# Kernel optimization log

Hardware: AMD Instinct MI355X
Metric: run time of the kernel (lower is better)

Reference implementation:

```python
import jax, jax.numpy as jnp
import numpy as np

EPS = 1e-05


def layer_norm(x, scale):
    # Faithful to source bug: returns scale * x_norm + scale (shift param unused)
    mean = jnp.mean(x, axis=-1, keepdims=True)
    var = jnp.var(x, axis=-1, keepdims=True)  # unbiased=False
    x_norm = (x - mean) / jnp.sqrt(var + EPS)
    return scale * x_norm + scale


def mhsa(x, wq, wk, wv, wo, bo, n_heads):
    b, t, d = x.shape
    hd = d // n_heads
    # torch Linear: y = x @ W.T (no qkv bias)
    q = (x @ wq.T).reshape(b, t, n_heads, hd).transpose(0, 2, 1, 3)  # bhtd
    k = (x @ wk.T).reshape(b, t, n_heads, hd).transpose(0, 2, 1, 3)
    v = (x @ wv.T).reshape(b, t, n_heads, hd).transpose(0, 2, 1, 3)
    scores = jnp.einsum('bhqd,bhkd->bhqk', q, k)
    causal = jnp.triu(jnp.ones((t, t), dtype=bool), k=1)
    scores = jnp.where(causal, -jnp.inf, scores)
    attn = jax.nn.softmax(scores / np.sqrt(hd).astype(np.float32), axis=-1)
    ctx = jnp.einsum('bhqk,bhkd->bhqd', attn, v)
    ctx = ctx.transpose(0, 2, 1, 3).reshape(b, t, d)
    return ctx @ wo.T + bo


def setup_inputs() -> dict:
    key = jax.random.key(0)
    ks = jax.random.split(key, 6)
    B, T, D = 2, 2048, 1024
    return {
        'x': jax.random.normal(ks[0], (B, T, D), dtype=jnp.float32),
        'wq': jax.random.normal(ks[1], (D, D), dtype=jnp.float32) * 0.02,
        'wk': jax.random.normal(ks[2], (D, D), dtype=jnp.float32) * 0.02,
        'wv': jax.random.normal(ks[3], (D, D), dtype=jnp.float32) * 0.02,
        'wo': jax.random.normal(ks[4], (D, D), dtype=jnp.float32) * 0.02,
        'bo': jnp.zeros((D,), dtype=jnp.float32),
        'ln1_scale': jnp.ones((D,), dtype=jnp.float32),
        'ln2_scale': jnp.ones((D,), dtype=jnp.float32),
    }


def reference(x, wq, wk, wv, wo, bo, ln1_scale, ln2_scale):
    n_heads = 16
    # Block 1: norm1 -> attn -> (+residual); dropout is identity in eval mode
    h = x + mhsa(layer_norm(x, ln1_scale), wq, wk, wv, wo, bo, n_heads)
    # Block 2: source calls self.attn (same weights) again, not self.ff
    out = h + mhsa(layer_norm(h, ln2_scale), wq, wk, wv, wo, bo, n_heads)
    return out
```

## Files before the change

kernel.cpp:

```cpp
#include <hip/hip_runtime.h>
#include <hip/hip_bf16.h>
#include <math.h>

#define Dm 1024
#define Tm 2048
#define Bm 2
#define Hm 16
#define HDm 64
#define Rm (Bm*Tm)
#define QS 3072

typedef __attribute__((ext_vector_type(8))) short sh8;
typedef __attribute__((ext_vector_type(4))) float f32x4;

#define AS1(p) ((const __attribute__((address_space(1))) void*)(p))
#define AS3(p) ((__attribute__((address_space(3))) void*)(p))

__device__ __forceinline__ short f2bs(float f) {
    union { float f; unsigned u; } v; v.f = f;
    unsigned r = v.u + 0x7FFFu + ((v.u >> 16) & 1u);
    return (short)(r >> 16);
}

__global__ __launch_bounds__(256) void convert_w(const float* __restrict__ wq,
                                                 const float* __restrict__ wk,
                                                 const float* __restrict__ wv,
                                                 const float* __restrict__ wo,
                                                 short* __restrict__ wqkv,
                                                 short* __restrict__ wob) {
    int idx = (blockIdx.x * 256 + threadIdx.x) * 4;
    const int M1 = 1 << 20;
    const float* src; short* dst; int off;
    if (idx < M1)           { src = wq; dst = wqkv;          off = idx; }
    else if (idx < 2*M1)    { src = wk; dst = wqkv + M1;     off = idx - M1; }
    else if (idx < 3*M1)    { src = wv; dst = wqkv + 2*M1;   off = idx - 2*M1; }
    else                    { src = wo; dst = wob;           off = idx - 3*M1; }
    float4 v = *(const float4*)(src + off);
    short4 o;
    o.x = f2bs(v.x); o.y = f2bs(v.y); o.z = f2bs(v.z); o.w = f2bs(v.w);
    *(short4*)(dst + off) = o;
}

__global__ __launch_bounds__(256) void ln_kernel(const float* __restrict__ x,
                                                 const float* __restrict__ scale,
                                                 short* __restrict__ out) {
    int row = blockIdx.x;
    int t = threadIdx.x;
    const float4* xr = (const float4*)(x + (size_t)row * Dm);
    float4 v = xr[t];
    float s  = v.x + v.y + v.z + v.w;
    float ss = v.x*v.x + v.y*v.y + v.z*v.z + v.w*v.w;
    #pragma unroll
    for (int off = 32; off; off >>= 1) {
        s  += __shfl_xor(s, off);
        ss += __shfl_xor(ss, off);
    }
    __shared__ float red[8];
    int wave = t >> 6, lane = t & 63;
    if (lane == 0) { red[wave*2] = s; red[wave*2+1] = ss; }
    __syncthreads();
    s  = red[0] + red[2] + red[4] + red[6];
    ss = red[1] + red[3] + red[5] + red[7];
    float mean = s * (1.0f / Dm);
    float var  = ss * (1.0f / Dm) - mean * mean;
    float rstd = 1.0f / sqrtf(var + 1e-5f);
    float4 sc = ((const float4*)scale)[t];
    short4 o;
    o.x = f2bs(sc.x * ((v.x - mean) * rstd) + sc.x);
    o.y = f2bs(sc.y * ((v.y - mean) * rstd) + sc.y);
    o.z = f2bs(sc.z * ((v.z - mean) * rstd) + sc.z);
    o.w = f2bs(sc.w * ((v.w - mean) * rstd) + sc.w);
    ((short4*)(out + (size_t)row * Dm))[t] = o;
}

template<int BN, bool BF16OUT>
__global__ __launch_bounds__(256) void gemm_mfma(const short* __restrict__ A,
                                                 const short* __restrict__ B,
                                                 const float* __restrict__ bias,
                                                 const float* __restrict__ res,
                                                 void* __restrict__ Cv,
                                                 int M, int N, int K) {
    __shared__ short As[128*32];
    __shared__ short Bs[BN*32];
    const int NJ = BN / 32;
    int t = threadIdx.x;
    int lane = t & 63, w = t >> 6;
    int l = lane & 15, quad = lane >> 4;
    int wm = (w & 1) * 64, wn = (w >> 1) * (BN/2);
    int m0 = blockIdx.y * 128, n0 = blockIdx.x * BN;

    f32x4 acc[4][NJ];
    #pragma unroll
    for (int i = 0; i < 4; i++)
        #pragma unroll
        for (int j = 0; j < NJ; j++)
            acc[i][j] = (f32x4){0.f,0.f,0.f,0.f};

    for (int k0 = 0; k0 < K; k0 += 32) {
        __syncthreads();
        #pragma unroll
        for (int p = 0; p < 2; p++) {
            int off = p*4096 + t*16;
            int row = off >> 6;
            int c = ((off >> 4) & 3) ^ (row & 3);
            const short* ga = A + (size_t)(m0 + row) * K + k0 + c*8;
            __builtin_amdgcn_global_load_lds(AS1(ga), AS3((char*)As + off), 16, 0, 0);
        }
        #pragma unroll
        for (int p = 0; p < BN/64; p++) {
            int off = p*4096 + t*16;
            int row = off >> 6;
            int c = ((off >> 4) & 3) ^ (row & 3);
            const short* gb = B + (size_t)(n0 + row) * K + k0 + c*8;
            __builtin_amdgcn_global_load_lds(AS1(gb), AS3((char*)Bs + off), 16, 0, 0);
        }
        __syncthreads();
        sh8 af[4], bf[NJ];
        #pragma unroll
        for (int i = 0; i < 4; i++) {
            int m = wm + i*16 + l;
            af[i] = *(const sh8*)((const char*)As + m*64 + ((quad ^ (m & 3)) * 16));
        }
        #pragma unroll
        for (int j = 0; j < NJ; j++) {
            int n = wn + j*16 + l;
            bf[j] = *(const sh8*)((const char*)Bs + n*64 + ((quad ^ (n & 3)) * 16));
        }
        #pragma unroll
        for (int i = 0; i < 4; i++)
            #pragma unroll
            for (int j = 0; j < NJ; j++)
                acc[i][j] = __builtin_amdgcn_mfma_f32_16x16x32_bf16(af[i], bf[j], acc[i][j], 0, 0, 0);
    }
    #pragma unroll
    for (int i = 0; i < 4; i++) {
        #pragma unroll
        for (int j = 0; j < NJ; j++) {
            #pragma unroll
            for (int r = 0; r < 4; r++) {
                int m = m0 + wm + i*16 + quad*4 + r;
                int n = n0 + wn + j*16 + l;
                float vv = acc[i][j][r];
                if (BF16OUT) {
                    ((short*)Cv)[(size_t)m * N + n] = f2bs(vv);
                } else {
                    vv += bias[n] + res[(size_t)m * N + n];
                    ((float*)Cv)[(size_t)m * N + n] = vv;
                }
            }
        }
    }
}

#define KP 72

__global__ __launch_bounds__(256) void attn_mfma(const short* __restrict__ qkv,
                                                 short* __restrict__ ctx) {
    __shared__ short Kl[64*64];
    __shared__ short Vt[64*KP];
    __shared__ short Pl[4][16*KP];
    int t = threadIdx.x;
    int lane = t & 63, w = t >> 6;
    int l = lane & 15, quad = lane >> 4;
    int pair = blockIdx.x;
    int bh = blockIdx.y;
    int b = bh >> 4, h = bh & 15;
    size_t rbase = (size_t)b * Tm;
    const short* qp0 = qkv + rbase * QS + h*HDm;
    const short* kp0 = qp0 + Dm;
    const short* vp0 = qp0 + 2*Dm;

    for (int ph = 0; ph < 2; ph++) {
        int qt = ph ? (31 - pair) : pair;
        int qtbase = qt * 64;

        sh8 qf0, qf1;
        {
            const short* qp = qp0 + (size_t)(qtbase + w*16 + l) * QS + quad*8;
            qf0 = *(const sh8*)qp;
            qf1 = *(const sh8*)(qp + 32);
        }
        f32x4 O[4] = {{0,0,0,0},{0,0,0,0},{0,0,0,0},{0,0,0,0}};
        float psum = 0.f;

        for (int kc = 0; kc <= qt; kc++) {
            int kbase = kc * 64;
            __syncthreads();
            #pragma unroll
            for (int p = 0; p < 2; p++) {
                int off = p*4096 + t*16;
                int key = off >> 7;
                int c = ((off >> 4) & 7) ^ (key & 7);
                const short* g = kp0 + (size_t)(kbase + key) * QS + c*8;
                __builtin_amdgcn_global_load_lds(AS1(g), AS3((char*)Kl + off), 16, 0, 0);
            }
            {
                int d = t & 63;
                const short* vp = vp0 + (size_t)(kbase + w*16) * QS + d;
                sh8 t0, t1;
                #pragma unroll
                for (int i = 0; i < 8; i++) t0[i] = vp[(size_t)i * QS];
                #pragma unroll
                for (int i = 0; i < 8; i++) t1[i] = vp[(size_t)(i+8) * QS];
                *(sh8*)&Vt[d*KP + w*16]     = t0;
                *(sh8*)&Vt[d*KP + w*16 + 8] = t1;
            }
            __syncthreads();

            f32x4 S[4];
            #pragma unroll
            for (int kt = 0; kt < 4; kt++) {
                const f32x4 z = {0.f,0.f,0.f,0.f};
                int key = kt*16 + l;
                const char* kb = (const char*)Kl + key*128;
                int sw = key & 7;
                sh8 k0 = *(const sh8*)(kb + ((quad ^ sw) * 16));
                sh8 k1 = *(const sh8*)(kb + (((4 + quad) ^ sw) * 16));
                f32x4 s = __builtin_amdgcn_mfma_f32_16x16x32_bf16(k0, qf0, z, 0, 0, 0);
                s = __builtin_amdgcn_mfma_f32_16x16x32_bf16(k1, qf1, s, 0, 0, 0);
                S[kt] = s;
            }
            bool needmask = (kbase + 63 > qtbase + w*16);
            int qrow = qtbase + w*16 + l;
            #pragma unroll
            for (int kt = 0; kt < 4; kt++) {
                float p[4];
                if (needmask) {
                    #pragma unroll
                    for (int r = 0; r < 4; r++) {
                        int key = kbase + kt*16 + quad*4 + r;
                        p[r] = (key > qrow) ? 0.f : __expf(S[kt][r] * 0.125f);
                        psum += p[r];
                    }
                } else {
                    #pragma unroll
                    for (int r = 0; r < 4; r++) {
                        p[r] = __expf(S[kt][r] * 0.125f);
                        psum += p[r];
                    }
                }
                __hip_bfloat162 pa = __float22bfloat162_rn({p[0], p[1]});
                __hip_bfloat162 pb = __float22bfloat162_rn({p[2], p[3]});
                union { __hip_bfloat162 h[2]; short4 s4; } u;
                u.h[0] = pa; u.h[1] = pb;
                *(short4*)&Pl[w][l*KP + kt*16 + quad*4] = u.s4;
            }
            sh8 p0 = *(const sh8*)&Pl[w][l*KP + quad*8];
            sh8 p1 = *(const sh8*)&Pl[w][l*KP + 32 + quad*8];
            #pragma unroll
            for (int dt = 0; dt < 4; dt++) {
                sh8 v0 = *(const sh8*)&Vt[(dt*16+l)*KP + quad*8];
                sh8 v1 = *(const sh8*)&Vt[(dt*16+l)*KP + 32 + quad*8];
                O[dt] = __builtin_amdgcn_mfma_f32_16x16x32_bf16(p0, v0, O[dt], 0, 0, 0);
                O[dt] = __builtin_amdgcn_mfma_f32_16x16x32_bf16(p1, v1, O[dt], 0, 0, 0);
            }
        }
        psum += __shfl_xor(psum, 16);
        psum += __shfl_xor(psum, 32);
        #pragma unroll
        for (int r = 0; r < 4; r++) {
            int src = (lane & 48) | (((lane >> 4) << 2) + r);
            float inv = 1.0f / __shfl(psum, src);
            int row = qtbase + w*16 + quad*4 + r;
            #pragma unroll
            for (int dt = 0; dt < 4; dt++)
                ctx[(rbase + row) * Dm + h*HDm + dt*16 + l] = f2bs(O[dt][r] * inv);
        }
    }
}

extern "C" void kernel_launch(void* const* d_in, const int* in_sizes, int n_in,
                              void* d_out, int out_size, void* d_ws, size_t ws_size,
                              hipStream_t stream) {
    const float* x   = (const float*)d_in[0];
    const float* wq  = (const float*)d_in[1];
    const float* wk  = (const float*)d_in[2];
    const float* wv  = (const float*)d_in[3];
    const float* wo  = (const float*)d_in[4];
    const float* bo  = (const float*)d_in[5];
    const float* ln1 = (const float*)d_in[6];
    const float* ln2 = (const float*)d_in[7];
    float* out = (float*)d_out;

    short* lnb  = (short*)d_ws;
    short* ctxb = lnb + (size_t)Rm*Dm;
    short* qkv  = ctxb + (size_t)Rm*Dm;
    short* wqkv = qkv + (size_t)Rm*QS;
    short* wob  = wqkv + (size_t)3*Dm*Dm;

    dim3 qgrid(QS/128, Rm/128);
    dim3 pgrid(Dm/64,  Rm/128);
    dim3 agrid(16, Bm*Hm);

    convert_w<<<4096, 256, 0, stream>>>(wq, wk, wv, wo, wqkv, wob);

    ln_kernel<<<Rm, 256, 0, stream>>>(x, ln1, lnb);
    gemm_mfma<128, true><<<qgrid, 256, 0, stream>>>(lnb, wqkv, nullptr, nullptr, qkv, Rm, QS, Dm);
    attn_mfma<<<agrid, 256, 0, stream>>>(qkv, ctxb);
    gemm_mfma<64, false><<<pgrid, 256, 0, stream>>>(ctxb, wob, bo, x, out, Rm, Dm, Dm);

    ln_kernel<<<Rm, 256, 0, stream>>>(out, ln2, lnb);
    gemm_mfma<128, true><<<qgrid, 256, 0, stream>>>(lnb, wqkv, nullptr, nullptr, qkv, Rm, QS, Dm);
    attn_mfma<<<agrid, 256, 0, stream>>>(qkv, ctxb);
    gemm_mfma<64, false><<<pgrid, 256, 0, stream>>>(ctxb, wob, bo, out, out, Rm, Dm, Dm);
}
```

Baseline: 330.8 us.

## Double-buffer K/V tiles in attention and launch one query tile per block

```diff
diff --git a/kernel.cpp b/kernel.cpp
--- a/kernel.cpp
+++ b/kernel.cpp
@@ -156,116 +156,138 @@
 
 __global__ __launch_bounds__(256) void attn_mfma(const short* __restrict__ qkv,
                                                  short* __restrict__ ctx) {
-    __shared__ short Kl[64*64];
-    __shared__ short Vt[64*KP];
+    __shared__ short Kl[2][64*64];
+    __shared__ short Vt[2][64*KP];
     __shared__ short Pl[4][16*KP];
     int t = threadIdx.x;
     int lane = t & 63, w = t >> 6;
     int l = lane & 15, quad = lane >> 4;
-    int pair = blockIdx.x;
+    int qt = 31 - (int)blockIdx.x;
     int bh = blockIdx.y;
     int b = bh >> 4, h = bh & 15;
     size_t rbase = (size_t)b * Tm;
     const short* qp0 = qkv + rbase * QS + h*HDm;
     const short* kp0 = qp0 + Dm;
     const short* vp0 = qp0 + 2*Dm;
-
-    for (int ph = 0; ph < 2; ph++) {
-        int qt = ph ? (31 - pair) : pair;
-        int qtbase = qt * 64;
-
-        sh8 qf0, qf1;
-        {
-            const short* qp = qp0 + (size_t)(qtbase + w*16 + l) * QS + quad*8;
-            qf0 = *(const sh8*)qp;
-            qf1 = *(const sh8*)(qp + 32);
-        }
-        f32x4 O[4] = {{0,0,0,0},{0,0,0,0},{0,0,0,0},{0,0,0,0}};
-        float psum = 0.f;
-
-        for (int kc = 0; kc <= qt; kc++) {
-            int kbase = kc * 64;
-            __syncthreads();
+    int qtbase = qt * 64;
+    int nch = qt + 1;
+
+    sh8 qf0, qf1;
+    {
+        const short* qp = qp0 + (size_t)(qtbase + w*16 + l) * QS + quad*8;
+        qf0 = *(const sh8*)qp;
+        qf1 = *(const sh8*)(qp + 32);
+    }
+    f32x4 O[4] = {{0,0,0,0},{0,0,0,0},{0,0,0,0},{0,0,0,0}};
+    float ps[4] = {0.f, 0.f, 0.f, 0.f};
+
+    int d = t & 63;
+    sh8 tv0, tv1;
+
+    {
+        #pragma unroll
+        for (int p = 0; p < 2; p++) {
+            int off = p*4096 + t*16;
+            int key = off >> 7;
+            int c = ((off >> 4) & 7) ^ (key & 7);
+            const short* g = kp0 + (size_t)key * QS + c*8;
+            __builtin_amdgcn_global_load_lds(AS1(g), AS3((char*)Kl[0] + off), 16, 0, 0);
+        }
+        const short* vp = vp0 + (size_t)(w*16) * QS + d;
+        #pragma unroll
+        for (int i = 0; i < 8; i++) tv0[i] = vp[(size_t)i * QS];
+        #pragma unroll
+        for (int i = 0; i < 8; i++) tv1[i] = vp[(size_t)(i+8) * QS];
+        *(sh8*)&Vt[0][d*KP + w*16]     = tv0;
+        *(sh8*)&Vt[0][d*KP + w*16 + 8] = tv1;
+    }
+    __syncthreads();
+
+    for (int kc = 0; kc < nch; kc++) {
+        int cur = kc & 1, nxt = cur ^ 1;
+        int kbase = kc * 64;
+        bool pf = (kc + 1 < nch);
+
+        if (pf) {
             #pragma unroll
             for (int p = 0; p < 2; p++) {
                 int off = p*4096 + t*16;
                 int key = off >> 7;
                 int c = ((off >> 4) & 7) ^ (key & 7);
-                const short* g = kp0 + (size_t)(kbase + key) * QS + c*8;
-                __builtin_amdgcn_global_load_lds(AS1(g), AS3((char*)Kl + off), 16, 0, 0);
+                const short* g = kp0 + (size_t)(kbase + 64 + key) * QS + c*8;
+                __builtin_amdgcn_global_load_lds(AS1(g), AS3((char*)Kl[nxt] + off), 16, 0, 0);
             }
-            {
-                int d = t & 63;
-                const short* vp = vp0 + (size_t)(kbase + w*16) * QS + d;
-                sh8 t0, t1;
+            const short* vp = vp0 + (size_t)(kbase + 64 + w*16) * QS + d;
+            #pragma unroll
+            for (int i = 0; i < 8; i++) tv0[i] = vp[(size_t)i * QS];
+            #pragma unroll
+            for (int i = 0; i < 8; i++) tv1[i] = vp[(size_t)(i+8) * QS];
+        }
+
+        f32x4 S[4];
+        #pragma unroll
+        for (int kt = 0; kt < 4; kt++) {
+            const f32x4 z = {0.f,0.f,0.f,0.f};
+            int key = kt*16 + l;
+            const char* kb = (const char*)Kl[cur] + key*128;
+            int sw = key & 7;
+            sh8 k0 = *(const sh8*)(kb + ((quad ^ sw) * 16));
+            sh8 k1 = *(const sh8*)(kb + (((4 + quad) ^ sw) * 16));
+            f32x4 s = __builtin_amdgcn_mfma_f32_16x16x32_bf16(k0, qf0, z, 0, 0, 0);
+            s = __builtin_amdgcn_mfma_f32_16x16x32_bf16(k1, qf1, s, 0, 0, 0);
+            S[kt] = s;
+        }
+        bool needmask = (kbase + 63 > qtbase + w*16);
+        int qrow = qtbase + w*16 + l;
+        #pragma unroll
+        for (int kt = 0; kt < 4; kt++) {
+            float p[4];
+            if (needmask) {
                 #pragma unroll
-                for (int i = 0; i < 8; i++) t0[i] = vp[(size_t)i * QS];
+                for (int r = 0; r < 4; r++) {
+                    int key = kbase + kt*16 + quad*4 + r;
+                    p[r] = (key > qrow) ? 0.f : __expf(S[kt][r] * 0.125f);
+                }
+            } else {
                 #pragma unroll
-                for (int i = 0; i < 8; i++) t1[i] = vp[(size_t)(i+8) * QS];
-                *(sh8*)&Vt[d*KP + w*16]     = t0;
-                *(sh8*)&Vt[d*KP + w*16 + 8] = t1;
+                for (int r = 0; r < 4; r++)
+                    p[r] = __expf(S[kt][r] * 0.125f);
             }
-            __syncthreads();
-
-            f32x4 S[4];
-            #pragma unroll
-            for (int kt = 0; kt < 4; kt++) {
-                const f32x4 z = {0.f,0.f,0.f,0.f};
-                int key = kt*16 + l;
-                const char* kb = (const char*)Kl + key*128;
-                int sw = key & 7;
-                sh8 k0 = *(const sh8*)(kb + ((quad ^ sw) * 16));
-                sh8 k1 = *(const sh8*)(kb + (((4 + quad) ^ sw) * 16));
-                f32x4 s = __builtin_amdgcn_mfma_f32_16x16x32_bf16(k0, qf0, z, 0, 0, 0);
-                s = __builtin_amdgcn_mfma_f32_16x16x32_bf16(k1, qf1, s, 0, 0, 0);
-                S[kt] = s;
-            }
-            bool needmask = (kbase + 63 > qtbase + w*16);
-            int qrow = qtbase + w*16 + l;
-            #pragma unroll
-            for (int kt = 0; kt < 4; kt++) {
-                float p[4];
-                if (needmask) {
-                    #pragma unroll
-                    for (int r = 0; r < 4; r++) {
-                        int key = kbase + kt*16 + quad*4 + r;
-                        p[r] = (key > qrow) ? 0.f : __expf(S[kt][r] * 0.125f);
-                        psum += p[r];
-                    }
-                } else {
-                    #pragma unroll
-                    for (int r = 0; r < 4; r++) {
-                        p[r] = __expf(S[kt][r] * 0.125f);
-                        psum += p[r];
-                    }
-                }
-                __hip_bfloat162 pa = __float22bfloat162_rn({p[0], p[1]});
-                __hip_bfloat162 pb = __float22bfloat162_rn({p[2], p[3]});
-                union { __hip_bfloat162 h[2]; short4 s4; } u;
-                u.h[0] = pa; u.h[1] = pb;
-                *(short4*)&Pl[w][l*KP + kt*16 + quad*4] = u.s4;
-            }
-            sh8 p0 = *(const sh8*)&Pl[w][l*KP + quad*8];
-            sh8 p1 = *(const sh8*)&Pl[w][l*KP + 32 + quad*8];
-            #pragma unroll
-            for (int dt = 0; dt < 4; dt++) {
-                sh8 v0 = *(const sh8*)&Vt[(dt*16+l)*KP + quad*8];
-                sh8 v1 = *(const sh8*)&Vt[(dt*16+l)*KP + 32 + quad*8];
-                O[dt] = __builtin_amdgcn_mfma_f32_16x16x32_bf16(p0, v0, O[dt], 0, 0, 0);
-                O[dt] = __builtin_amdgcn_mfma_f32_16x16x32_bf16(p1, v1, O[dt], 0, 0, 0);
-            }
-        }
-        psum += __shfl_xor(psum, 16);
-        psum += __shfl_xor(psum, 32);
-        #pragma unroll
-        for (int r = 0; r < 4; r++) {
-            int src = (lane & 48) | (((lane >> 4) << 2) + r);
-            float inv = 1.0f / __shfl(psum, src);
-            int row = qtbase + w*16 + quad*4 + r;
-            #pragma unroll
-            for (int dt = 0; dt < 4; dt++)
-                ctx[(rbase + row) * Dm + h*HDm + dt*16 + l] = f2bs(O[dt][r] * inv);
-        }
+            ps[kt] += (p[0] + p[1]) + (p[2] + p[3]);
+            __hip_bfloat162 pa = __float22bfloat162_rn({p[0], p[1]});
+            __hip_bfloat162 pb = __float22bfloat162_rn({p[2], p[3]});
+            union { __hip_bfloat162 h[2]; short4 s4; } u;
+            u.h[0] = pa; u.h[1] = pb;
+            *(short4*)&Pl[w][l*KP + kt*16 + quad*4] = u.s4;
+        }
+        sh8 p0 = *(const sh8*)&Pl[w][l*KP + quad*8];
+        sh8 p1 = *(const sh8*)&Pl[w][l*KP + 32 + quad*8];
+        #pragma unroll
+        for (int dt = 0; dt < 4; dt++) {
+            sh8 v0 = *(const sh8*)&Vt[cur][(dt*16+l)*KP + quad*8];
+            sh8 v1 = *(const sh8*)&Vt[cur][(dt*16+l)*KP + 32 + quad*8];
+            O[dt] = __builtin_amdgcn_mfma_f32_16x16x32_bf16(p0, v0, O[dt], 0, 0, 0);
+            O[dt] = __builtin_amdgcn_mfma_f32_16x16x32_bf16(p1, v1, O[dt], 0, 0, 0);
+        }
+
+        if (pf) {
+            *(sh8*)&Vt[nxt][d*KP + w*16]     = tv0;
+            *(sh8*)&Vt[nxt][d*KP + w*16 + 8] = tv1;
+        }
+        __syncthreads();
+    }
+
+    float psum = (ps[0] + ps[1]) + (ps[2] + ps[3]);
+    psum += __shfl_xor(psum, 16);
+    psum += __shfl_xor(psum, 32);
+    #pragma unroll
+    for (int r = 0; r < 4; r++) {
+        int src = (lane & 48) | (((lane >> 4) << 2) + r);
+        float inv = 1.0f / __shfl(psum, src);
+        int row = qtbase + w*16 + quad*4 + r;
+        #pragma unroll
+        for (int dt = 0; dt < 4; dt++)
+            ctx[(rbase + row) * Dm + h*HDm + dt*16 + l] = f2bs(O[dt][r] * inv);
     }
 }
 
@@ -290,7 +312,7 @@
 
     dim3 qgrid(QS/128, Rm/128);
     dim3 pgrid(Dm/64,  Rm/128);
-    dim3 agrid(16, Bm*Hm);
+    dim3 agrid(32, Bm*Hm);
 
     convert_w<<<4096, 256, 0, stream>>>(wq, wk, wv, wo, wqkv, wob);
 
```

Result: slower. 407.2 us (+23.1%).

## Write V transposed from QKV GEMM and double-buffer K/V staging in attention

Applied to the files above, without the earlier changes.

```diff
diff --git a/kernel.cpp b/kernel.cpp
--- a/kernel.cpp
+++ b/kernel.cpp
@@ -8,7 +8,7 @@
 #define Hm 16
 #define HDm 64
 #define Rm (Bm*Tm)
-#define QS 3072
+#define QKS 2048
 
 typedef __attribute__((ext_vector_type(8))) short sh8;
 typedef __attribute__((ext_vector_type(4))) float f32x4;
@@ -73,15 +73,17 @@
     ((short4*)(out + (size_t)row * Dm))[t] = o;
 }
 
-template<int BN, bool BF16OUT>
+template<int BN, int MODE>
 __global__ __launch_bounds__(256) void gemm_mfma(const short* __restrict__ A,
                                                  const short* __restrict__ B,
                                                  const float* __restrict__ bias,
                                                  const float* __restrict__ res,
                                                  void* __restrict__ Cv,
+                                                 short* __restrict__ Vt,
                                                  int M, int N, int K) {
     __shared__ short As[128*32];
     __shared__ short Bs[BN*32];
+    __shared__ short Tb[(MODE==1) ? 4*16*68 : 4];
     const int NJ = BN / 32;
     int t = threadIdx.x;
     int lane = t & 63, w = t >> 6;
@@ -132,21 +134,51 @@
             for (int j = 0; j < NJ; j++)
                 acc[i][j] = __builtin_amdgcn_mfma_f32_16x16x32_bf16(af[i], bf[j], acc[i][j], 0, 0, 0);
     }
-    #pragma unroll
-    for (int i = 0; i < 4; i++) {
-        #pragma unroll
-        for (int j = 0; j < NJ; j++) {
-            #pragma unroll
-            for (int r = 0; r < 4; r++) {
-                int m = m0 + wm + i*16 + quad*4 + r;
-                int n = n0 + wn + j*16 + l;
-                float vv = acc[i][j][r];
-                if (BF16OUT) {
-                    ((short*)Cv)[(size_t)m * N + n] = f2bs(vv);
-                } else {
-                    vv += bias[n] + res[(size_t)m * N + n];
+    if (MODE == 0) {
+        #pragma unroll
+        for (int i = 0; i < 4; i++)
+            #pragma unroll
+            for (int j = 0; j < NJ; j++)
+                #pragma unroll
+                for (int r = 0; r < 4; r++) {
+                    int m = m0 + wm + i*16 + quad*4 + r;
+                    int n = n0 + wn + j*16 + l;
+                    float vv = acc[i][j][r] + bias[n] + res[(size_t)m * N + n];
                     ((float*)Cv)[(size_t)m * N + n] = vv;
                 }
+    } else {
+        if (n0 < 2048) {
+            #pragma unroll
+            for (int i = 0; i < 4; i++)
+                #pragma unroll
+                for (int j = 0; j < NJ; j++)
+                    #pragma unroll
+                    for (int r = 0; r < 4; r++) {
+                        int m = m0 + wm + i*16 + quad*4 + r;
+                        int n = n0 + wn + j*16 + l;
+                        ((short*)Cv)[(size_t)m * QKS + n] = f2bs(acc[i][j][r]);
+                    }
+        } else {
+            int bq = m0 >> 11;
+            int key0 = (m0 & 2047) + wm;
+            int h = (n0 + wn - 2048) >> 6;
+            short* vout = Vt + ((size_t)(bq*Hm + h) * HDm) * Tm + key0;
+            #pragma unroll
+            for (int j = 0; j < NJ; j++) {
+                #pragma unroll
+                for (int i = 0; i < 4; i++) {
+                    short4 o;
+                    o.x = f2bs(acc[i][j][0]); o.y = f2bs(acc[i][j][1]);
+                    o.z = f2bs(acc[i][j][2]); o.w = f2bs(acc[i][j][3]);
+                    *(short4*)&Tb[w*(16*68) + l*68 + i*16 + quad*4] = o;
+                }
+                #pragma unroll
+                for (int st = 0; st < 2; st++) {
+                    int rr = st*8 + (lane >> 3);
+                    int cc = lane & 7;
+                    sh8 vv = *(const sh8*)&Tb[w*(16*68) + rr*68 + cc*8];
+                    *(sh8*)(vout + (size_t)(j*16 + rr) * Tm + cc*8) = vv;
+                }
             }
         }
     }
@@ -154,10 +186,25 @@
 
 #define KP 72
 
-__global__ __launch_bounds__(256) void attn_mfma(const short* __restrict__ qkv,
+__device__ __forceinline__ void stage_kv(const short* kp0, const short* vh,
+                                         int kbase, short* Kd, short* Vd, int t) {
+    #pragma unroll
+    for (int p = 0; p < 2; p++) {
+        int off = p*4096 + t*16;
+        int row = off >> 7;
+        int c = ((off >> 4) & 7) ^ (row & 7);
+        const short* gk = kp0 + (size_t)(kbase + row) * QKS + c*8;
+        __builtin_amdgcn_global_load_lds(AS1(gk), AS3((char*)Kd + off), 16, 0, 0);
+        const short* gv = vh + (size_t)row * Tm + kbase + c*8;
+        __builtin_amdgcn_global_load_lds(AS1(gv), AS3((char*)Vd + off), 16, 0, 0);
+    }
+}
+
+__global__ __launch_bounds__(256) void attn_mfma(const short* __restrict__ qk,
+                                                 const short* __restrict__ vtg,
                                                  short* __restrict__ ctx) {
-    __shared__ short Kl[64*64];
-    __shared__ short Vt[64*KP];
+    __shared__ short Kl[2][64*64];
+    __shared__ short Vl[2][64*64];
     __shared__ short Pl[4][16*KP];
     int t = threadIdx.x;
     int lane = t & 63, w = t >> 6;
@@ -166,9 +213,13 @@
     int bh = blockIdx.y;
     int b = bh >> 4, h = bh & 15;
     size_t rbase = (size_t)b * Tm;
-    const short* qp0 = qkv + rbase * QS + h*HDm;
+    const short* qp0 = qk + rbase * QKS + h*HDm;
     const short* kp0 = qp0 + Dm;
-    const short* vp0 = qp0 + 2*Dm;
+    const short* vh  = vtg + ((size_t)bh * HDm) * Tm;
+
+    int cur = 0;
+    stage_kv(kp0, vh, 0, Kl[0], Vl[0], t);
+    __syncthreads();
 
     for (int ph = 0; ph < 2; ph++) {
         int qt = ph ? (31 - pair) : pair;
@@ -176,43 +227,27 @@
 
         sh8 qf0, qf1;
         {
-            const short* qp = qp0 + (size_t)(qtbase + w*16 + l) * QS + quad*8;
+            const short* qp = qp0 + (size_t)(qtbase + w*16 + l) * QKS + quad*8;
             qf0 = *(const sh8*)qp;
             qf1 = *(const sh8*)(qp + 32);
         }
         f32x4 O[4] = {{0,0,0,0},{0,0,0,0},{0,0,0,0},{0,0,0,0}};
-        float psum = 0.f;
+        float ps[4] = {0.f, 0.f, 0.f, 0.f};
 
         for (int kc = 0; kc <= qt; kc++) {
             int kbase = kc * 64;
-            __syncthreads();
-            #pragma unroll
-            for (int p = 0; p < 2; p++) {
-                int off = p*4096 + t*16;
-                int key = off >> 7;
-                int c = ((off >> 4) & 7) ^ (key & 7);
-                const short* g = kp0 + (size_t)(kbase + key) * QS + c*8;
-                __builtin_amdgcn_global_load_lds(AS1(g), AS3((char*)Kl + off), 16, 0, 0);
-            }
-            {
-                int d = t & 63;
-                const short* vp = vp0 + (size_t)(kbase + w*16) * QS + d;
-                sh8 t0, t1;
-                #pragma unroll
-                for (int i = 0; i < 8; i++) t0[i] = vp[(size_t)i * QS];
-                #pragma unroll
-                for (int i = 0; i < 8; i++) t1[i] = vp[(size_t)(i+8) * QS];
-                *(sh8*)&Vt[d*KP + w*16]     = t0;
-                *(sh8*)&Vt[d*KP + w*16 + 8] = t1;
-            }
-            __syncthreads();
+            bool last = (ph == 1) && (kc == qt);
+            if (!last) {
+                int nb = (kc < qt) ? kbase + 64 : 0;
+                stage_kv(kp0, vh, nb, Kl[cur^1], Vl[cur^1], t);
+            }
 
             f32x4 S[4];
             #pragma unroll
             for (int kt = 0; kt < 4; kt++) {
                 const f32x4 z = {0.f,0.f,0.f,0.f};
                 int key = kt*16 + l;
-                const char* kb = (const char*)Kl + key*128;
+                const char* kb = (const char*)Kl[cur] + key*128;
                 int sw = key & 7;
                 sh8 k0 = *(const sh8*)(kb + ((quad ^ sw) * 16));
                 sh8 k1 = *(const sh8*)(kb + (((4 + quad) ^ sw) * 16));
@@ -230,31 +265,36 @@
                     for (int r = 0; r < 4; r++) {
                         int key = kbase + kt*16 + quad*4 + r;
                         p[r] = (key > qrow) ? 0.f : __expf(S[kt][r] * 0.125f);
-                        psum += p[r];
                     }
                 } else {
                     #pragma unroll
-                    for (int r = 0; r < 4; r++) {
+                    for (int r = 0; r < 4; r++)
                         p[r] = __expf(S[kt][r] * 0.125f);
-                        psum += p[r];
-                    }
                 }
+                ps[kt] += (p[0] + p[1]) + (p[2] + p[3]);
                 __hip_bfloat162 pa = __float22bfloat162_rn({p[0], p[1]});
                 __hip_bfloat162 pb = __float22bfloat162_rn({p[2], p[3]});
-                union { __hip_bfloat162 h[2]; short4 s4; } u;
-                u.h[0] = pa; u.h[1] = pb;
+                union { __hip_bfloat162 hh[2]; short4 s4; } u;
+                u.hh[0] = pa; u.hh[1] = pb;
                 *(short4*)&Pl[w][l*KP + kt*16 + quad*4] = u.s4;
             }
             sh8 p0 = *(const sh8*)&Pl[w][l*KP + quad*8];
             sh8 p1 = *(const sh8*)&Pl[w][l*KP + 32 + quad*8];
             #pragma unroll
             for (int dt = 0; dt < 4; dt++) {
-                sh8 v0 = *(const sh8*)&Vt[(dt*16+l)*KP + quad*8];
-                sh8 v1 = *(const sh8*)&Vt[(dt*16+l)*KP + 32 + quad*8];
+                int d = dt*16 + l;
+                const char* vb = (const char*)Vl[cur] + d*128;
+                int sw = d & 7;
+                sh8 v0 = *(const sh8*)(vb + ((quad ^ sw) * 16));
+                sh8 v1 = *(const sh8*)(vb + (((4 + quad) ^ sw) * 16));
                 O[dt] = __builtin_amdgcn_mfma_f32_16x16x32_bf16(p0, v0, O[dt], 0, 0, 0);
                 O[dt] = __builtin_amdgcn_mfma_f32_16x16x32_bf16(p1, v1, O[dt], 0, 0, 0);
             }
-        }
+            __syncthreads();
+            cur ^= 1;
+        }
+
+        float psum = (ps[0] + ps[1]) + (ps[2] + ps[3]);
         psum += __shfl_xor(psum, 16);
         psum += __shfl_xor(psum, 32);
         #pragma unroll
@@ -283,24 +323,25 @@
     float* out = (float*)d_out;
 
     short* lnb  = (short*)d_ws;
-    short* ctxb = lnb + (size_t)Rm*Dm;
-    short* qkv  = ctxb + (size_t)Rm*Dm;
-    short* wqkv = qkv + (size_t)Rm*QS;
+    short* ctxb = lnb  + (size_t)Rm*Dm;
+    short* qk   = ctxb + (size_t)Rm*Dm;
+    short* vtg  = qk   + (size_t)Rm*QKS;
+    short* wqkv = vtg  + (size_t)Bm*Hm*HDm*Tm;
     short* wob  = wqkv + (size_t)3*Dm*Dm;
 
-    dim3 qgrid(QS/128, Rm/128);
-    dim3 pgrid(Dm/64,  Rm/128);
+    dim3 qgrid(3072/128, Rm/128);
+    dim3 pgrid(Dm/64,    Rm/128);
     dim3 agrid(16, Bm*Hm);
 
     convert_w<<<4096, 256, 0, stream>>>(wq, wk, wv, wo, wqkv, wob);
 
     ln_kernel<<<Rm, 256, 0, stream>>>(x, ln1, lnb);
-    gemm_mfma<128, true><<<qgrid, 256, 0, stream>>>(lnb, wqkv, nullptr, nullptr, qkv, Rm, QS, Dm);
-    attn_mfma<<<agrid, 256, 0, stream>>>(qkv, ctxb);
-    gemm_mfma<64, false><<<pgrid, 256, 0, stream>>>(ctxb, wob, bo, x, out, Rm, Dm, Dm);
+    gemm_mfma<128, 1><<<qgrid, 256, 0, stream>>>(lnb, wqkv, nullptr, nullptr, qk, vtg, Rm, 3072, Dm);
+    attn_mfma<<<agrid, 256, 0, stream>>>(qk, vtg, ctxb);
+    gemm_mfma<64, 0><<<pgrid, 256, 0, stream>>>(ctxb, wob, bo, x, out, nullptr, Rm, Dm, Dm);
 
     ln_kernel<<<Rm, 256, 0, stream>>>(out, ln2, lnb);
-    gemm_mfma<128, true><<<qgrid, 256, 0, stream>>>(lnb, wqkv, nullptr, nullptr, qkv, Rm, QS, Dm);
-    attn_mfma<<<agrid, 256, 0, stream>>>(qkv, ctxb);
-    gemm_mfma<64, false><<<pgrid, 256, 0, stream>>>(ctxb, wob, bo, out, out, Rm, Dm, Dm);
-}
+    gemm_mfma<128, 1><<<qgrid, 256, 0, stream>>>(lnb, wqkv, nullptr, nullptr, qk, vtg, Rm, 3072, Dm);
+    attn_mfma<<<agrid, 256, 0, stream>>>(qk, vtg, ctxb);
+    gemm_mfma<64, 0><<<pgrid, 256, 0, stream>>>(ctxb, wob, bo, out, out, nullptr, Rm, Dm, Dm);
+}
```

New measurement: 320.6 us. 3.1% less time.
